# Kernel optimization log

Hardware: AMD Instinct MI355X
Metric: run time of the kernel (lower is better)

The kernel has to match this reference:

```python
import jax, jax.numpy as jnp
import numpy as np

FP16_MAX = 65504.0  # clamp_fp16 bound
GROUP = 64          # SVDQuant int4 group size along in_features


def _int4_quant_dequant(w):
    """Symmetric per-(out_channel, group) int4 fake-quant of a weight [out, in].
    Emulates the W4 weight numerics of SVDQW4A4Linear at the dequantized level."""
    o, i = w.shape
    wg = w.reshape(o, i // GROUP, GROUP)
    scale = np.max(np.abs(wg), axis=-1, keepdims=True) / 7.0
    scale = np.where(scale == 0.0, 1.0, scale)
    q = np.clip(np.round(wg / scale), -8, 7)
    return (q * scale).reshape(o, i).astype(np.float32)


def setup_inputs() -> dict:
    dim, hidden = 3072, 8192
    B, S = 2, 4096
    rng = np.random.default_rng(0)
    # fused [w1; w3] weight: [2*hidden, dim]; down proj w2: [dim, hidden]
    w13 = _int4_quant_dequant((rng.standard_normal((2 * hidden, dim)) * 0.02).astype(np.float32))
    w2 = _int4_quant_dequant((rng.standard_normal((dim, hidden)) * 0.02).astype(np.float32))
    key = jax.random.key(0)
    x = jax.random.normal(key, (B, S, dim), dtype=jnp.float32)
    return {"x": x, "w13": jnp.asarray(w13), "w2": jnp.asarray(w2)}


def reference(x, w13, w2):
    # fused gate/up projection: [B,S,dim] @ [2H,dim]^T -> [B,S,2H]
    h = jnp.einsum("bsd,hd->bsh", x, w13)
    # NOTE: original code does `x3, x1 = x.chunk(2, dim=-1)` -> first half is x3
    x3, x1 = jnp.split(h, 2, axis=-1)
    g = jnp.clip(jax.nn.silu(x1) * x3, -FP16_MAX, FP16_MAX)  # clamp_fp16
    # down projection: [B,S,H] @ [dim,H]^T -> [B,S,dim]
    return jnp.einsum("bsh,dh->bsd", g, w2)
```

## Files before the change

### kernel.cpp

```cpp
#include <hip/hip_runtime.h>
#include <hip/hip_bf16.h>


typedef __attribute__((ext_vector_type(8))) __bf16 bf16x8;
typedef __attribute__((ext_vector_type(4))) float f32x4;

#define GLD_LDS16(gptr, lptr)                                                        \
  __builtin_amdgcn_global_load_lds(                                                  \
      (const __attribute__((address_space(1))) void*)(gptr),                         \
      (__attribute__((address_space(3))) void*)(lptr), 16, 0, 0)

#define VMCNT(n) asm volatile("s_waitcnt vmcnt(" #n ")" ::: "memory")
#define BAR_SYNC()                                          \
  do {                                                      \
    asm volatile("s_waitcnt lgkmcnt(0)" ::: "memory");      \
    __builtin_amdgcn_s_barrier();                           \
    asm volatile("" ::: "memory");                          \
  } while (0)
#define BAR_ONLY()                                          \
  do {                                                      \
    __builtin_amdgcn_s_barrier();                           \
    asm volatile("" ::: "memory");                          \
  } while (0)

__device__ __forceinline__ __bf16 bfr(float f) {
  unsigned int u = __builtin_bit_cast(unsigned int, f);
  unsigned short r = (unsigned short)((u + 0x7FFFu + ((u >> 16) & 1u)) >> 16);
  return __builtin_bit_cast(__bf16, r);
}

__global__ __launch_bounds__(256)
void k_cvt(const float* __restrict__ src, unsigned short* __restrict__ dst, long n) {
  long i = ((long)blockIdx.x * 256 + threadIdx.x) * 8;
  const long stride = (long)gridDim.x * 256 * 8;
  for (; i < n; i += stride) {
    float4 f0 = *(const float4*)(src + i);
    float4 f1 = *(const float4*)(src + i + 4);
    bf16x8 o;
    o[0] = bfr(f0.x); o[1] = bfr(f0.y); o[2] = bfr(f0.z); o[3] = bfr(f0.w);
    o[4] = bfr(f1.x); o[5] = bfr(f1.y); o[6] = bfr(f1.z); o[7] = bfr(f1.w);
    *(bf16x8*)(dst + i) = o;
  }
}

__global__ __launch_bounds__(512, 2)
void k_gateup8(const unsigned short* __restrict__ X,
               const unsigned short* __restrict__ W13,
               __hip_bfloat16* __restrict__ G)
{
  constexpr int K = 3072, LDG = 8192, NT = K / 64;
  __shared__ unsigned short lds[65536];

  const int t = threadIdx.x;
  const int lane = t & 63, wid = t >> 6;
  const int wm = wid >> 2, wn = wid & 3;
  const int l15 = lane & 15, lhi = lane >> 4, sw = l15 & 7;

  const int bid = blockIdx.x;
  const int swz = (bid & 7) * 256 + (bid >> 3);
  const int mb = swz >> 6, nb = swz & 63;

  const int srow = t >> 3;
  const int scol = ((t & 7) ^ (srow & 7)) * 8;
  const unsigned short* xa = X   + (size_t)(mb * 256 + srow) * K + scol;
  const unsigned short* b3 = W13 + (size_t)(nb * 128 + srow) * K + scol;
  const unsigned short* b1 = W13 + (size_t)(8192 + nb * 128 + srow) * K + scol;
  const int lo = t * 8;

  f32x4 acc3[8][2], acc1[8][2];
#pragma unroll
  for (int m = 0; m < 8; ++m)
#pragma unroll
    for (int n = 0; n < 2; ++n) {
      acc3[m][n] = (f32x4){0.f, 0.f, 0.f, 0.f};
      acc1[m][n] = (f32x4){0.f, 0.f, 0.f, 0.f};
    }

#pragma unroll
  for (int tt = 0; tt < 2; ++tt) {
    unsigned short* A  = lds + tt * 32768;
    unsigned short* B3 = A + 16384;
    unsigned short* B1 = A + 24576;
    const int kt = tt * 64;
#pragma unroll
    for (int q = 0; q < 4; ++q)
      GLD_LDS16(xa + (size_t)(q * 64) * K + kt, A + q * 4096 + lo);
#pragma unroll
    for (int r = 0; r < 2; ++r) {
      GLD_LDS16(b3 + (size_t)(r * 64) * K + kt, B3 + r * 4096 + lo);
      GLD_LDS16(b1 + (size_t)(r * 64) * K + kt, B1 + r * 4096 + lo);
    }
  }

  for (int tk = 0; tk < NT; ++tk) {
    unsigned short* A  = lds + (tk & 1) * 32768;
    unsigned short* B3 = A + 16384;
    unsigned short* B1 = A + 24576;
    const int ks = (tk + 2 < NT ? tk + 2 : 0) * 64;

    VMCNT(8);
    BAR_ONLY();

    bf16x8 ra[4][2], r3a[2], r1a[2], r3b[2], r1b[2];
#pragma unroll
    for (int m = 0; m < 4; ++m)
#pragma unroll
      for (int kk = 0; kk < 2; ++kk)
        ra[m][kk] = *(const bf16x8*)(A + (wm * 128 + m * 16 + l15) * 64 + ((kk * 4 + lhi) ^ sw) * 8);
#pragma unroll
    for (int kk = 0; kk < 2; ++kk) {
      r3a[kk] = *(const bf16x8*)(B3 + (wn * 32 + l15) * 64 + ((kk * 4 + lhi) ^ sw) * 8);
      r1a[kk] = *(const bf16x8*)(B1 + (wn * 32 + l15) * 64 + ((kk * 4 + lhi) ^ sw) * 8);
    }
    __builtin_amdgcn_s_setprio(1);
#pragma unroll
    for (int m = 0; m < 4; ++m)
#pragma unroll
      for (int kk = 0; kk < 2; ++kk) {
        acc3[m][0] = __builtin_amdgcn_mfma_f32_16x16x32_bf16(ra[m][kk], r3a[kk], acc3[m][0], 0, 0, 0);
        acc1[m][0] = __builtin_amdgcn_mfma_f32_16x16x32_bf16(ra[m][kk], r1a[kk], acc1[m][0], 0, 0, 0);
      }
    __builtin_amdgcn_s_setprio(0);
    BAR_SYNC();

    GLD_LDS16(xa + (size_t)(0 * 64) * K + ks, A + 0 * 4096 + lo);
    GLD_LDS16(xa + (size_t)(2 * 64) * K + ks, A + 2 * 4096 + lo);
#pragma unroll
    for (int kk = 0; kk < 2; ++kk) {
      r3b[kk] = *(const bf16x8*)(B3 + (wn * 32 + 16 + l15) * 64 + ((kk * 4 + lhi) ^ sw) * 8);
      r1b[kk] = *(const bf16x8*)(B1 + (wn * 32 + 16 + l15) * 64 + ((kk * 4 + lhi) ^ sw) * 8);
    }
    __builtin_amdgcn_s_setprio(1);
#pragma unroll
    for (int m = 0; m < 4; ++m)
#pragma unroll
      for (int kk = 0; kk < 2; ++kk) {
        acc3[m][1] = __builtin_amdgcn_mfma_f32_16x16x32_bf16(ra[m][kk], r3b[kk], acc3[m][1], 0, 0, 0);
        acc1[m][1] = __builtin_amdgcn_mfma_f32_16x16x32_bf16(ra[m][kk], r1b[kk], acc1[m][1], 0, 0, 0);
      }
    __builtin_amdgcn_s_setprio(0);
    BAR_SYNC();

#pragma unroll
    for (int r = 0; r < 2; ++r) {
      GLD_LDS16(b3 + (size_t)(r * 64) * K + ks, B3 + r * 4096 + lo);
      GLD_LDS16(b1 + (size_t)(r * 64) * K + ks, B1 + r * 4096 + lo);
    }
#pragma unroll
    for (int m = 0; m < 4; ++m)
#pragma unroll
      for (int kk = 0; kk < 2; ++kk)
        ra[m][kk] = *(const bf16x8*)(A + (wm * 128 + 64 + m * 16 + l15) * 64 + ((kk * 4 + lhi) ^ sw) * 8);
    __builtin_amdgcn_s_setprio(1);
#pragma unroll
    for (int m = 0; m < 4; ++m)
#pragma unroll
      for (int kk = 0; kk < 2; ++kk) {
        acc3[4 + m][0] = __builtin_amdgcn_mfma_f32_16x16x32_bf16(ra[m][kk], r3a[kk], acc3[4 + m][0], 0, 0, 0);
        acc1[4 + m][0] = __builtin_amdgcn_mfma_f32_16x16x32_bf16(ra[m][kk], r1a[kk], acc1[4 + m][0], 0, 0, 0);
      }
    __builtin_amdgcn_s_setprio(0);
    BAR_SYNC();

    GLD_LDS16(xa + (size_t)(1 * 64) * K + ks, A + 1 * 4096 + lo);
    GLD_LDS16(xa + (size_t)(3 * 64) * K + ks, A + 3 * 4096 + lo);
    __builtin_amdgcn_s_setprio(1);
#pragma unroll
    for (int m = 0; m < 4; ++m)
#pragma unroll
      for (int kk = 0; kk < 2; ++kk) {
        acc3[4 + m][1] = __builtin_amdgcn_mfma_f32_16x16x32_bf16(ra[m][kk], r3b[kk], acc3[4 + m][1], 0, 0, 0);
        acc1[4 + m][1] = __builtin_amdgcn_mfma_f32_16x16x32_bf16(ra[m][kk], r1b[kk], acc1[4 + m][1], 0, 0, 0);
      }
    __builtin_amdgcn_s_setprio(0);
  }

  const int gr0 = mb * 256 + wm * 128;
  const int gc0 = nb * 128 + wn * 32;
#pragma unroll
  for (int m = 0; m < 8; ++m)
#pragma unroll
    for (int n = 0; n < 2; ++n)
#pragma unroll
      for (int r = 0; r < 4; ++r) {
        float h3 = acc3[m][n][r];
        float h1 = acc1[m][n][r];
        float s  = h1 / (1.f + __expf(-h1));
        float g  = fminf(fmaxf(s * h3, -65504.f), 65504.f);
        G[(size_t)(gr0 + m * 16 + lhi * 4 + r) * LDG + (gc0 + n * 16 + l15)] =
            __float2bfloat16(g);
      }
}

__global__ __launch_bounds__(512, 2)
void k_down8(const unsigned short* __restrict__ Gm,
             const unsigned short* __restrict__ W2,
             float* __restrict__ Out)
{
  constexpr int K = 8192, LDO = 3072, NT = K / 64;
  __shared__ unsigned short lds[49152];

  const int t = threadIdx.x;
  const int lane = t & 63, wid = t >> 6;
  const int wm = wid >> 2, wn = wid & 3;
  const int l15 = lane & 15, lhi = lane >> 4, sw = l15 & 7;

  const int bid = blockIdx.x;
  const int swz = (bid & 7) * 96 + (bid >> 3);
  const int mb = swz / 24, nb = swz % 24;

  const int srow = t >> 3;
  const int scol = ((t & 7) ^ (srow & 7)) * 8;
  const unsigned short* ga = Gm + (size_t)(mb * 256 + srow) * K + scol;
  const unsigned short* wb = W2 + (size_t)(nb * 128 + srow) * K + scol;
  const int lo = t * 8;

  f32x4 acc[8][2];
#pragma unroll
  for (int m = 0; m < 8; ++m)
#pragma unroll
    for (int n = 0; n < 2; ++n)
      acc[m][n] = (f32x4){0.f, 0.f, 0.f, 0.f};

#pragma unroll
  for (int tt = 0; tt < 2; ++tt) {
    unsigned short* A = lds + tt * 24576;
    unsigned short* B = A + 16384;
    const int kt = tt * 64;
#pragma unroll
    for (int q = 0; q < 4; ++q)
      GLD_LDS16(ga + (size_t)(q * 64) * K + kt, A + q * 4096 + lo);
#pragma unroll
    for (int r = 0; r < 2; ++r)
      GLD_LDS16(wb + (size_t)(r * 64) * K + kt, B + r * 4096 + lo);
  }

  for (int tk = 0; tk < NT; ++tk) {
    unsigned short* A = lds + (tk & 1) * 24576;
    unsigned short* B = A + 16384;
    const int ks = (tk + 2 < NT ? tk + 2 : 0) * 64;

    VMCNT(6);
    BAR_ONLY();

    bf16x8 ra[4][2], rb[2][2];
#pragma unroll
    for (int m = 0; m < 4; ++m)
#pragma unroll
      for (int kk = 0; kk < 2; ++kk)
        ra[m][kk] = *(const bf16x8*)(A + (wm * 128 + m * 16 + l15) * 64 + ((kk * 4 + lhi) ^ sw) * 8);
#pragma unroll
    for (int n = 0; n < 2; ++n)
#pragma unroll
      for (int kk = 0; kk < 2; ++kk)
        rb[n][kk] = *(const bf16x8*)(B + (wn * 32 + n * 16 + l15) * 64 + ((kk * 4 + lhi) ^ sw) * 8);
    __builtin_amdgcn_s_setprio(1);
#pragma unroll
    for (int m = 0; m < 4; ++m)
#pragma unroll
      for (int n = 0; n < 2; ++n)
#pragma unroll
        for (int kk = 0; kk < 2; ++kk)
          acc[m][n] = __builtin_amdgcn_mfma_f32_16x16x32_bf16(ra[m][kk], rb[n][kk], acc[m][n], 0, 0, 0);
    __builtin_amdgcn_s_setprio(0);
    BAR_SYNC();

#pragma unroll
    for (int r = 0; r < 2; ++r)
      GLD_LDS16(wb + (size_t)(r * 64) * K + ks, B + r * 4096 + lo);
    GLD_LDS16(ga + (size_t)(0 * 64) * K + ks, A + 0 * 4096 + lo);
    GLD_LDS16(ga + (size_t)(2 * 64) * K + ks, A + 2 * 4096 + lo);
#pragma unroll
    for (int m = 0; m < 4; ++m)
#pragma unroll
      for (int kk = 0; kk < 2; ++kk)
        ra[m][kk] = *(const bf16x8*)(A + (wm * 128 + 64 + m * 16 + l15) * 64 + ((kk * 4 + lhi) ^ sw) * 8);
    __builtin_amdgcn_s_setprio(1);
#pragma unroll
    for (int m = 0; m < 4; ++m)
#pragma unroll
      for (int n = 0; n < 2; ++n)
#pragma unroll
        for (int kk = 0; kk < 2; ++kk)
          acc[4 + m][n] = __builtin_amdgcn_mfma_f32_16x16x32_bf16(ra[m][kk], rb[n][kk], acc[4 + m][n], 0, 0, 0);
    __builtin_amdgcn_s_setprio(0);
    BAR_SYNC();
    GLD_LDS16(ga + (size_t)(1 * 64) * K + ks, A + 1 * 4096 + lo);
    GLD_LDS16(ga + (size_t)(3 * 64) * K + ks, A + 3 * 4096 + lo);
  }

  const int r0 = mb * 256 + wm * 128;
  const int c0 = nb * 128 + wn * 32;
#pragma unroll
  for (int m = 0; m < 8; ++m)
#pragma unroll
    for (int n = 0; n < 2; ++n)
#pragma unroll
      for (int r = 0; r < 4; ++r)
        Out[(size_t)(r0 + m * 16 + lhi * 4 + r) * LDO + (c0 + n * 16 + l15)] =
            acc[m][n][r];
}

extern "C" void kernel_launch(void* const* d_in, const int* in_sizes, int n_in,
                              void* d_out, int out_size, void* d_ws, size_t ws_size,
                              hipStream_t stream) {
  const float* x   = (const float*)d_in[0];
  const float* w13 = (const float*)d_in[1];
  const float* w2  = (const float*)d_in[2];
  float* out = (float*)d_out;

  const long NX = 25165824L, NW13 = 50331648L, NW2 = 25165824L;
  const size_t XB = 50331648, W13B = 100663296, W2B = 50331648;

  unsigned short* xb   = (unsigned short*)d_ws;
  unsigned short* w13b = (unsigned short*)((char*)d_ws + XB);
  unsigned short* w2b  = (unsigned short*)((char*)d_ws + XB + W13B);
  __hip_bfloat16* g    = (__hip_bfloat16*)((char*)d_ws + XB + W13B + W2B);

  k_cvt<<<2048, 256, 0, stream>>>(x,   xb,   NX);
  k_cvt<<<2048, 256, 0, stream>>>(w13, w13b, NW13);
  k_cvt<<<2048, 256, 0, stream>>>(w2,  w2b,  NW2);
  k_gateup8<<<2048, 512, 0, stream>>>(xb, w13b, g);
  k_down8<<<768, 512, 0, stream>>>((const unsigned short*)g, w2b, out);
}
```

Before: 1.200 ms.

## Switch both GEMMs to 32x32x16 MFMA with deeper LDS pipelining

Both GEMM kernels now use 32x32x16 bf16 MFMA tiles instead of 16x16x32. The gate/up kernel gets a 4-stage LDS ring with a K-step of 32, and the down kernel gets a 3-stage ring with a new 4x2 wave layout of 64x64 tiles per wave. Each K iteration now has one barrier instead of several split phases. The aim is fewer LDS reads per flop and fewer barriers. In exchange, register and LDS pressure rise, and dropping the lgkmcnt wait before the barrier slightly weakens the ordering of reads against overwrites.

```diff
diff --git a/kernel.cpp b/kernel.cpp
--- a/kernel.cpp
+++ b/kernel.cpp
@@ -3,7 +3,7 @@
 
 
 typedef __attribute__((ext_vector_type(8))) __bf16 bf16x8;
-typedef __attribute__((ext_vector_type(4))) float f32x4;
+typedef __attribute__((ext_vector_type(16))) float f32x16;
 
 #define GLD_LDS16(gptr, lptr)                                                        \
   __builtin_amdgcn_global_load_lds(                                                  \
@@ -11,17 +11,7 @@
       (__attribute__((address_space(3))) void*)(lptr), 16, 0, 0)
 
 #define VMCNT(n) asm volatile("s_waitcnt vmcnt(" #n ")" ::: "memory")
-#define BAR_SYNC()                                          \
-  do {                                                      \
-    asm volatile("s_waitcnt lgkmcnt(0)" ::: "memory");      \
-    __builtin_amdgcn_s_barrier();                           \
-    asm volatile("" ::: "memory");                          \
-  } while (0)
-#define BAR_ONLY()                                          \
-  do {                                                      \
-    __builtin_amdgcn_s_barrier();                           \
-    asm volatile("" ::: "memory");                          \
-  } while (0)
+#define FENCE()  asm volatile("" ::: "memory")
 
 __device__ __forceinline__ __bf16 bfr(float f) {
   unsigned int u = __builtin_bit_cast(unsigned int, f);
@@ -44,166 +34,114 @@
 }
 
 __global__ __launch_bounds__(512, 2)
-void k_gateup8(const unsigned short* __restrict__ X,
-               const unsigned short* __restrict__ W13,
-               __hip_bfloat16* __restrict__ G)
+void k_gateup10(const unsigned short* __restrict__ X,
+                const unsigned short* __restrict__ W13,
+                __hip_bfloat16* __restrict__ G)
 {
-  constexpr int K = 3072, LDG = 8192, NT = K / 64;
-  __shared__ unsigned short lds[65536];
+  constexpr int K = 3072, LDG = 8192, NT = K / 32;
+  __shared__ unsigned short lds[4 * 16384];
 
   const int t = threadIdx.x;
-  const int lane = t & 63, wid = t >> 6;
+  const int l = t & 63, wid = t >> 6;
   const int wm = wid >> 2, wn = wid & 3;
-  const int l15 = lane & 15, lhi = lane >> 4, sw = l15 & 7;
+  const int l31 = l & 31, lh = l >> 5;
+  const int sw2 = (l31 >> 1) & 3;
 
   const int bid = blockIdx.x;
   const int swz = (bid & 7) * 256 + (bid >> 3);
   const int mb = swz >> 6, nb = swz & 63;
 
-  const int srow = t >> 3;
-  const int scol = ((t & 7) ^ (srow & 7)) * 8;
+  const int srow = t >> 2;
+  const int scol = ((t & 3) ^ ((srow >> 1) & 3)) * 8;
   const unsigned short* xa = X   + (size_t)(mb * 256 + srow) * K + scol;
   const unsigned short* b3 = W13 + (size_t)(nb * 128 + srow) * K + scol;
   const unsigned short* b1 = W13 + (size_t)(8192 + nb * 128 + srow) * K + scol;
   const int lo = t * 8;
 
-  f32x4 acc3[8][2], acc1[8][2];
-#pragma unroll
-  for (int m = 0; m < 8; ++m)
-#pragma unroll
-    for (int n = 0; n < 2; ++n) {
-      acc3[m][n] = (f32x4){0.f, 0.f, 0.f, 0.f};
-      acc1[m][n] = (f32x4){0.f, 0.f, 0.f, 0.f};
+  f32x16 acc3[4], acc1[4];
+#pragma unroll
+  for (int mf = 0; mf < 4; ++mf)
+#pragma unroll
+    for (int r = 0; r < 16; ++r) { acc3[mf][r] = 0.f; acc1[mf][r] = 0.f; }
+
+#pragma unroll
+  for (int tt = 0; tt < 3; ++tt) {
+    unsigned short* S = lds + tt * 16384;
+    const int kt = tt * 32;
+    GLD_LDS16(xa + kt, S + lo);
+    GLD_LDS16(xa + (size_t)128 * K + kt, S + 4096 + lo);
+    GLD_LDS16(b3 + kt, S + 8192 + lo);
+    GLD_LDS16(b1 + kt, S + 12288 + lo);
+  }
+
+  for (int tk = 0; tk < NT; ++tk) {
+    unsigned short* A = lds + (tk & 3) * 16384;
+    unsigned short* S = lds + ((tk + 3) & 3) * 16384;
+    const int ksrc = (tk + 3 < NT ? tk + 3 : 0) * 32;
+
+    VMCNT(8);
+    __builtin_amdgcn_s_barrier();
+    FENCE();
+
+    bf16x8 ra[4][2], r3[2], r1[2];
+#pragma unroll
+    for (int mf = 0; mf < 4; ++mf)
+#pragma unroll
+      for (int ks = 0; ks < 2; ++ks) {
+        const int row = wm * 128 + mf * 32 + l31;
+        ra[mf][ks] = *(const bf16x8*)(A + row * 32 + (((ks * 2 + lh) ^ sw2) * 8));
+      }
+#pragma unroll
+    for (int ks = 0; ks < 2; ++ks) {
+      const int row = wn * 32 + l31;
+      const int sl = ((ks * 2 + lh) ^ sw2) * 8;
+      r3[ks] = *(const bf16x8*)(A + 8192 + row * 32 + sl);
+      r1[ks] = *(const bf16x8*)(A + 12288 + row * 32 + sl);
     }
 
-#pragma unroll
-  for (int tt = 0; tt < 2; ++tt) {
-    unsigned short* A  = lds + tt * 32768;
-    unsigned short* B3 = A + 16384;
-    unsigned short* B1 = A + 24576;
-    const int kt = tt * 64;
-#pragma unroll
-    for (int q = 0; q < 4; ++q)
-      GLD_LDS16(xa + (size_t)(q * 64) * K + kt, A + q * 4096 + lo);
-#pragma unroll
-    for (int r = 0; r < 2; ++r) {
-      GLD_LDS16(b3 + (size_t)(r * 64) * K + kt, B3 + r * 4096 + lo);
-      GLD_LDS16(b1 + (size_t)(r * 64) * K + kt, B1 + r * 4096 + lo);
+    GLD_LDS16(xa + ksrc, S + lo);
+    GLD_LDS16(xa + (size_t)128 * K + ksrc, S + 4096 + lo);
+    GLD_LDS16(b3 + ksrc, S + 8192 + lo);
+    GLD_LDS16(b1 + ksrc, S + 12288 + lo);
+
+    __builtin_amdgcn_s_setprio(1);
+#pragma unroll
+    for (int ks = 0; ks < 2; ++ks)
+#pragma unroll
+      for (int mf = 0; mf < 4; ++mf) {
+        acc3[mf] = __builtin_amdgcn_mfma_f32_32x32x16_bf16(ra[mf][ks], r3[ks], acc3[mf], 0, 0, 0);
+        acc1[mf] = __builtin_amdgcn_mfma_f32_32x32x16_bf16(ra[mf][ks], r1[ks], acc1[mf], 0, 0, 0);
+      }
+    __builtin_amdgcn_s_setprio(0);
+  }
+
+  const int gr0 = mb * 256 + wm * 128;
+  const int gc  = nb * 128 + wn * 32 + l31;
+#pragma unroll
+  for (int mf = 0; mf < 4; ++mf)
+#pragma unroll
+    for (int r = 0; r < 16; ++r) {
+      const int row = gr0 + mf * 32 + (r & 3) + 8 * (r >> 2) + 4 * lh;
+      float h3 = acc3[mf][r], h1 = acc1[mf][r];
+      float s  = h1 / (1.f + __expf(-h1));
+      float g  = fminf(fmaxf(s * h3, -65504.f), 65504.f);
+      G[(size_t)row * LDG + gc] = __float2bfloat16(g);
     }
-  }
-
-  for (int tk = 0; tk < NT; ++tk) {
-    unsigned short* A  = lds + (tk & 1) * 32768;
-    unsigned short* B3 = A + 16384;
-    unsigned short* B1 = A + 24576;
-    const int ks = (tk + 2 < NT ? tk + 2 : 0) * 64;
-
-    VMCNT(8);
-    BAR_ONLY();
-
-    bf16x8 ra[4][2], r3a[2], r1a[2], r3b[2], r1b[2];
-#pragma unroll
-    for (int m = 0; m < 4; ++m)
-#pragma unroll
-      for (int kk = 0; kk < 2; ++kk)
-        ra[m][kk] = *(const bf16x8*)(A + (wm * 128 + m * 16 + l15) * 64 + ((kk * 4 + lhi) ^ sw) * 8);
-#pragma unroll
-    for (int kk = 0; kk < 2; ++kk) {
-      r3a[kk] = *(const bf16x8*)(B3 + (wn * 32 + l15) * 64 + ((kk * 4 + lhi) ^ sw) * 8);
-      r1a[kk] = *(const bf16x8*)(B1 + (wn * 32 + l15) * 64 + ((kk * 4 + lhi) ^ sw) * 8);
-    }
-    __builtin_amdgcn_s_setprio(1);
-#pragma unroll
-    for (int m = 0; m < 4; ++m)
-#pragma unroll
-      for (int kk = 0; kk < 2; ++kk) {
-        acc3[m][0] = __builtin_amdgcn_mfma_f32_16x16x32_bf16(ra[m][kk], r3a[kk], acc3[m][0], 0, 0, 0);
-        acc1[m][0] = __builtin_amdgcn_mfma_f32_16x16x32_bf16(ra[m][kk], r1a[kk], acc1[m][0], 0, 0, 0);
-      }
-    __builtin_amdgcn_s_setprio(0);
-    BAR_SYNC();
-
-    GLD_LDS16(xa + (size_t)(0 * 64) * K + ks, A + 0 * 4096 + lo);
-    GLD_LDS16(xa + (size_t)(2 * 64) * K + ks, A + 2 * 4096 + lo);
-#pragma unroll
-    for (int kk = 0; kk < 2; ++kk) {
-      r3b[kk] = *(const bf16x8*)(B3 + (wn * 32 + 16 + l15) * 64 + ((kk * 4 + lhi) ^ sw) * 8);
-      r1b[kk] = *(const bf16x8*)(B1 + (wn * 32 + 16 + l15) * 64 + ((kk * 4 + lhi) ^ sw) * 8);
-    }
-    __builtin_amdgcn_s_setprio(1);
-#pragma unroll
-    for (int m = 0; m < 4; ++m)
-#pragma unroll
-      for (int kk = 0; kk < 2; ++kk) {
-        acc3[m][1] = __builtin_amdgcn_mfma_f32_16x16x32_bf16(ra[m][kk], r3b[kk], acc3[m][1], 0, 0, 0);
-        acc1[m][1] = __builtin_amdgcn_mfma_f32_16x16x32_bf16(ra[m][kk], r1b[kk], acc1[m][1], 0, 0, 0);
-      }
-    __builtin_amdgcn_s_setprio(0);
-    BAR_SYNC();
-
-#pragma unroll
-    for (int r = 0; r < 2; ++r) {
-      GLD_LDS16(b3 + (size_t)(r * 64) * K + ks, B3 + r * 4096 + lo);
-      GLD_LDS16(b1 + (size_t)(r * 64) * K + ks, B1 + r * 4096 + lo);
-    }
-#pragma unroll
-    for (int m = 0; m < 4; ++m)
-#pragma unroll
-      for (int kk = 0; kk < 2; ++kk)
-        ra[m][kk] = *(const bf16x8*)(A + (wm * 128 + 64 + m * 16 + l15) * 64 + ((kk * 4 + lhi) ^ sw) * 8);
-    __builtin_amdgcn_s_setprio(1);
-#pragma unroll
-    for (int m = 0; m < 4; ++m)
-#pragma unroll
-      for (int kk = 0; kk < 2; ++kk) {
-        acc3[4 + m][0] = __builtin_amdgcn_mfma_f32_16x16x32_bf16(ra[m][kk], r3a[kk], acc3[4 + m][0], 0, 0, 0);
-        acc1[4 + m][0] = __builtin_amdgcn_mfma_f32_16x16x32_bf16(ra[m][kk], r1a[kk], acc1[4 + m][0], 0, 0, 0);
-      }
-    __builtin_amdgcn_s_setprio(0);
-    BAR_SYNC();
-
-    GLD_LDS16(xa + (size_t)(1 * 64) * K + ks, A + 1 * 4096 + lo);
-    GLD_LDS16(xa + (size_t)(3 * 64) * K + ks, A + 3 * 4096 + lo);
-    __builtin_amdgcn_s_setprio(1);
-#pragma unroll
-    for (int m = 0; m < 4; ++m)
-#pragma unroll
-      for (int kk = 0; kk < 2; ++kk) {
-        acc3[4 + m][1] = __builtin_amdgcn_mfma_f32_16x16x32_bf16(ra[m][kk], r3b[kk], acc3[4 + m][1], 0, 0, 0);
-        acc1[4 + m][1] = __builtin_amdgcn_mfma_f32_16x16x32_bf16(ra[m][kk], r1b[kk], acc1[4 + m][1], 0, 0, 0);
-      }
-    __builtin_amdgcn_s_setprio(0);
-  }
-
-  const int gr0 = mb * 256 + wm * 128;
-  const int gc0 = nb * 128 + wn * 32;
-#pragma unroll
-  for (int m = 0; m < 8; ++m)
-#pragma unroll
-    for (int n = 0; n < 2; ++n)
-#pragma unroll
-      for (int r = 0; r < 4; ++r) {
-        float h3 = acc3[m][n][r];
-        float h1 = acc1[m][n][r];
-        float s  = h1 / (1.f + __expf(-h1));
-        float g  = fminf(fmaxf(s * h3, -65504.f), 65504.f);
-        G[(size_t)(gr0 + m * 16 + lhi * 4 + r) * LDG + (gc0 + n * 16 + l15)] =
-            __float2bfloat16(g);
-      }
 }
 
 __global__ __launch_bounds__(512, 2)
-void k_down8(const unsigned short* __restrict__ Gm,
-             const unsigned short* __restrict__ W2,
-             float* __restrict__ Out)
+void k_down10(const unsigned short* __restrict__ Gm,
+              const unsigned short* __restrict__ W2,
+              float* __restrict__ Out)
 {
   constexpr int K = 8192, LDO = 3072, NT = K / 64;
-  __shared__ unsigned short lds[49152];
+  __shared__ unsigned short lds[3 * 24576];
 
   const int t = threadIdx.x;
-  const int lane = t & 63, wid = t >> 6;
-  const int wm = wid >> 2, wn = wid & 3;
-  const int l15 = lane & 15, lhi = lane >> 4, sw = l15 & 7;
+  const int l = t & 63, wid = t >> 6;
+  const int wm = wid >> 1, wn = wid & 1;
+  const int l31 = l & 31, lh = l >> 5;
+  const int sw = l31 & 7;
 
   const int bid = blockIdx.x;
   const int swz = (bid & 7) * 96 + (bid >> 3);
@@ -215,90 +153,80 @@
   const unsigned short* wb = W2 + (size_t)(nb * 128 + srow) * K + scol;
   const int lo = t * 8;
 
-  f32x4 acc[8][2];
-#pragma unroll
-  for (int m = 0; m < 8; ++m)
-#pragma unroll
-    for (int n = 0; n < 2; ++n)
-      acc[m][n] = (f32x4){0.f, 0.f, 0.f, 0.f};
+  f32x16 acc[2][2];
+#pragma unroll
+  for (int mf = 0; mf < 2; ++mf)
+#pragma unroll
+    for (int nf = 0; nf < 2; ++nf)
+#pragma unroll
+      for (int r = 0; r < 16; ++r) acc[mf][nf][r] = 0.f;
 
 #pragma unroll
   for (int tt = 0; tt < 2; ++tt) {
-    unsigned short* A = lds + tt * 24576;
-    unsigned short* B = A + 16384;
+    unsigned short* S = lds + tt * 24576;
     const int kt = tt * 64;
 #pragma unroll
     for (int q = 0; q < 4; ++q)
-      GLD_LDS16(ga + (size_t)(q * 64) * K + kt, A + q * 4096 + lo);
-#pragma unroll
-    for (int r = 0; r < 2; ++r)
-      GLD_LDS16(wb + (size_t)(r * 64) * K + kt, B + r * 4096 + lo);
+      GLD_LDS16(ga + (size_t)(q * 64) * K + kt, S + q * 4096 + lo);
+#pragma unroll
+    for (int h = 0; h < 2; ++h)
+      GLD_LDS16(wb + (size_t)(h * 64) * K + kt, S + 16384 + h * 4096 + lo);
   }
 
   for (int tk = 0; tk < NT; ++tk) {
-    unsigned short* A = lds + (tk & 1) * 24576;
-    unsigned short* B = A + 16384;
-    const int ks = (tk + 2 < NT ? tk + 2 : 0) * 64;
+    unsigned short* A = lds + (tk % 3) * 24576;
+    unsigned short* S = lds + ((tk + 2) % 3) * 24576;
+    const int ksrc = (tk + 2 < NT ? tk + 2 : 0) * 64;
 
     VMCNT(6);
-    BAR_ONLY();
-
-    bf16x8 ra[4][2], rb[2][2];
-#pragma unroll
-    for (int m = 0; m < 4; ++m)
-#pragma unroll
-      for (int kk = 0; kk < 2; ++kk)
-        ra[m][kk] = *(const bf16x8*)(A + (wm * 128 + m * 16 + l15) * 64 + ((kk * 4 + lhi) ^ sw) * 8);
-#pragma unroll
-    for (int n = 0; n < 2; ++n)
-#pragma unroll
-      for (int kk = 0; kk < 2; ++kk)
-        rb[n][kk] = *(const bf16x8*)(B + (wn * 32 + n * 16 + l15) * 64 + ((kk * 4 + lhi) ^ sw) * 8);
+    __builtin_amdgcn_s_barrier();
+    FENCE();
+
+    bf16x8 ra[2][4], rb[2][4];
+#pragma unroll
+    for (int mf = 0; mf < 2; ++mf)
+#pragma unroll
+      for (int ks = 0; ks < 4; ++ks) {
+        const int row = wm * 64 + mf * 32 + l31;
+        ra[mf][ks] = *(const bf16x8*)(A + row * 64 + (((ks * 2 + lh) ^ sw) * 8));
+      }
+#pragma unroll
+    for (int nf = 0; nf < 2; ++nf)
+#pragma unroll
+      for (int ks = 0; ks < 4; ++ks) {
+        const int row = wn * 64 + nf * 32 + l31;
+        rb[nf][ks] = *(const bf16x8*)(A + 16384 + row * 64 + (((ks * 2 + lh) ^ sw) * 8));
+      }
+
+#pragma unroll
+    for (int q = 0; q < 4; ++q)
+      GLD_LDS16(ga + (size_t)(q * 64) * K + ksrc, S + q * 4096 + lo);
+#pragma unroll
+    for (int h = 0; h < 2; ++h)
+      GLD_LDS16(wb + (size_t)(h * 64) * K + ksrc, S + 16384 + h * 4096 + lo);
+
     __builtin_amdgcn_s_setprio(1);
 #pragma unroll
-    for (int m = 0; m < 4; ++m)
-#pragma unroll
-      for (int n = 0; n < 2; ++n)
-#pragma unroll
-        for (int kk = 0; kk < 2; ++kk)
-          acc[m][n] = __builtin_amdgcn_mfma_f32_16x16x32_bf16(ra[m][kk], rb[n][kk], acc[m][n], 0, 0, 0);
+    for (int ks = 0; ks < 4; ++ks)
+#pragma unroll
+      for (int mf = 0; mf < 2; ++mf)
+#pragma unroll
+        for (int nf = 0; nf < 2; ++nf)
+          acc[mf][nf] = __builtin_amdgcn_mfma_f32_32x32x16_bf16(ra[mf][ks], rb[nf][ks], acc[mf][nf], 0, 0, 0);
     __builtin_amdgcn_s_setprio(0);
-    BAR_SYNC();
-
-#pragma unroll
-    for (int r = 0; r < 2; ++r)
-      GLD_LDS16(wb + (size_t)(r * 64) * K + ks, B + r * 4096 + lo);
-    GLD_LDS16(ga + (size_t)(0 * 64) * K + ks, A + 0 * 4096 + lo);
-    GLD_LDS16(ga + (size_t)(2 * 64) * K + ks, A + 2 * 4096 + lo);
-#pragma unroll
-    for (int m = 0; m < 4; ++m)
-#pragma unroll
-      for (int kk = 0; kk < 2; ++kk)
-        ra[m][kk] = *(const bf16x8*)(A + (wm * 128 + 64 + m * 16 + l15) * 64 + ((kk * 4 + lhi) ^ sw) * 8);
-    __builtin_amdgcn_s_setprio(1);
-#pragma unroll
-    for (int m = 0; m < 4; ++m)
-#pragma unroll
-      for (int n = 0; n < 2; ++n)
-#pragma unroll
-        for (int kk = 0; kk < 2; ++kk)
-          acc[4 + m][n] = __builtin_amdgcn_mfma_f32_16x16x32_bf16(ra[m][kk], rb[n][kk], acc[4 + m][n], 0, 0, 0);
-    __builtin_amdgcn_s_setprio(0);
-    BAR_SYNC();
-    GLD_LDS16(ga + (size_t)(1 * 64) * K + ks, A + 1 * 4096 + lo);
-    GLD_LDS16(ga + (size_t)(3 * 64) * K + ks, A + 3 * 4096 + lo);
-  }
-
-  const int r0 = mb * 256 + wm * 128;
-  const int c0 = nb * 128 + wn * 32;
-#pragma unroll
-  for (int m = 0; m < 8; ++m)
-#pragma unroll
-    for (int n = 0; n < 2; ++n)
-#pragma unroll
-      for (int r = 0; r < 4; ++r)
-        Out[(size_t)(r0 + m * 16 + lhi * 4 + r) * LDO + (c0 + n * 16 + l15)] =
-            acc[m][n][r];
+  }
+
+  const int r0 = mb * 256 + wm * 64;
+  const int c0 = nb * 128 + wn * 64;
+#pragma unroll
+  for (int mf = 0; mf < 2; ++mf)
+#pragma unroll
+    for (int nf = 0; nf < 2; ++nf)
+#pragma unroll
+      for (int r = 0; r < 16; ++r) {
+        const int row = r0 + mf * 32 + (r & 3) + 8 * (r >> 2) + 4 * lh;
+        Out[(size_t)row * LDO + c0 + nf * 32 + l31] = acc[mf][nf][r];
+      }
 }
 
 extern "C" void kernel_launch(void* const* d_in, const int* in_sizes, int n_in,
@@ -320,6 +248,6 @@
   k_cvt<<<2048, 256, 0, stream>>>(x,   xb,   NX);
   k_cvt<<<2048, 256, 0, stream>>>(w13, w13b, NW13);
   k_cvt<<<2048, 256, 0, stream>>>(w2,  w2b,  NW2);
-  k_gateup8<<<2048, 512, 0, stream>>>(xb, w13b, g);
-  k_down8<<<768, 512, 0, stream>>>((const unsigned short*)g, w2b, out);
-}
+  k_gateup10<<<2048, 512, 0, stream>>>(xb, w13b, g);
+  k_down10<<<768, 512, 0, stream>>>((const unsigned short*)g, w2b, out);
+}
```

After: 1.348 ms. 12.3% more time.
